# Performance work log

Measured on AMD Instinct MI355X. Metric: run time of the kernel, lower is better.

The kernel has to match this reference:

```python
import jax, jax.numpy as jnp
import numpy as np

N_HEAD = 16


def setup_inputs() -> dict:
    key = jax.random.key(0)
    k1, k2, k3 = jax.random.split(key, 3)
    B, T, N = 4, 2048, 1024
    x = jax.random.normal(k1, (B, T, N), dtype=jnp.float32)
    W_attn = jax.random.normal(k2, (N, 3 * N), dtype=jnp.float32) * (1.0 / np.sqrt(N))
    b_attn = jnp.zeros((3 * N,), dtype=jnp.float32)
    W_proj = jax.random.normal(k3, (N, N), dtype=jnp.float32) * (1.0 / np.sqrt(N))
    b_proj = jnp.zeros((N,), dtype=jnp.float32)
    return {"x": x, "W_attn": W_attn, "b_attn": b_attn, "W_proj": W_proj, "b_proj": b_proj}


def reference(x, W_attn, b_attn, W_proj, b_proj):
    B, T, N = x.shape
    H = N_HEAD
    Dh = N // H
    qkv = x @ W_attn + b_attn                      # [B, T, 3N]
    q, k, v = jnp.split(qkv, 3, axis=2)
    # [B, H, T, Dh]
    q = q.reshape(B, T, H, Dh).transpose(0, 2, 1, 3)
    k = k.reshape(B, T, H, Dh).transpose(0, 2, 1, 3)
    v = v.reshape(B, T, H, Dh).transpose(0, 2, 1, 3)
    att = jnp.einsum('bhqd,bhkd->bhqk', q, k) / (Dh ** 0.5)
    mask = jnp.tril(jnp.ones((T, T), dtype=bool))
    att = jnp.where(mask[None, None], att, jnp.finfo(x.dtype).min)
    att = jax.nn.softmax(att, axis=-1)
    y = jnp.einsum('bhqk,bhkd->bhqd', att, v)      # [B, H, T, Dh]
    y = y.transpose(0, 2, 1, 3).reshape(B, T, N)
    return y @ W_proj + b_proj
```

## Files before the change

kernel.cpp:

```cpp
#include <hip/hip_runtime.h>
#include <hip/hip_bf16.h>


typedef __attribute__((ext_vector_type(8))) short short8;
typedef __attribute__((ext_vector_type(4))) float f32x4;

#define MFMA16(a, b, c) __builtin_amdgcn_mfma_f32_16x16x32_bf16((a), (b), (c), 0, 0, 0)

#if defined(__has_builtin)
#if __has_builtin(__builtin_amdgcn_exp2f)
#define EXP2(x) __builtin_amdgcn_exp2f(x)
#endif
#endif
#ifndef EXP2
#define EXP2(x) exp2f(x)
#endif

__device__ __forceinline__ void gload_lds16(const void* g, void* l) {
  __builtin_amdgcn_global_load_lds(
      (const __attribute__((address_space(1))) unsigned int*)g,
      (__attribute__((address_space(3))) unsigned int*)l, 16, 0, 0);
}

__device__ __forceinline__ unsigned pack_bf16x2(float lo, float hi) {
  unsigned ulo = __float_as_uint(lo) + 0x8000u;
  unsigned uhi = __float_as_uint(hi) + 0x8000u;
  return __builtin_amdgcn_perm(uhi, ulo, 0x07060302u);
}

__device__ __forceinline__ unsigned short bf16u(float f) {
  return (unsigned short)((__float_as_uint(f) + 0x8000u) >> 16);
}

__global__ void conv_f32_bf16(const float* __restrict__ src,
                              unsigned* __restrict__ dst, int n4) {
  int i = blockIdx.x * blockDim.x + threadIdx.x;
  if (i >= n4) return;
  float4 v = ((const float4*)src)[i];
  uint2 o;
  o.x = pack_bf16x2(v.x, v.y);
  o.y = pack_bf16x2(v.z, v.w);
  ((uint2*)dst)[i] = o;
}

__global__ void transpose_bf16(const float* __restrict__ src,
                               __hip_bfloat16* __restrict__ dst, int R, int C) {
  __shared__ float tile[32][33];
  int tx = threadIdx.x, ty = threadIdx.y;
  int c0 = blockIdx.x * 32, r0 = blockIdx.y * 32;
#pragma unroll
  for (int i = 0; i < 32; i += 8)
    tile[ty + i][tx] = src[(long)(r0 + ty + i) * C + c0 + tx];
  __syncthreads();
#pragma unroll
  for (int i = 0; i < 32; i += 8)
    dst[(long)(c0 + ty + i) * R + r0 + tx] = __float2bfloat16(tile[tx][ty + i]);
}

template <int EPI>
__global__ __launch_bounds__(256, 2) void gemm_bt(
    const __hip_bfloat16* __restrict__ A, const __hip_bfloat16* __restrict__ Bt,
    const float* __restrict__ bias, void* o0, void* o1, void* o2, int N, int K) {
  __shared__ alignas(16) char smem[34816];
  short8 (*As)[8] = (short8(*)[8])smem;
  short8 (*Bs)[8] = (short8(*)[8])(smem + 16384);
  unsigned short (*C16)[136] = (unsigned short(*)[136])smem;
  float (*C32)[132] = (float(*)[132])smem;

  const int tid = threadIdx.x;
  const int lane = tid & 63, w = tid >> 6;
  const int l15 = lane & 15, quad = lane >> 4;
  const int wm = (w >> 1) * 64, wn = (w & 1) * 64;
  const int rowBase = blockIdx.y * 128;
  const int colBase = blockIdx.x * 128;
  const int sr8 = lane >> 3;
  const int scc = (lane & 7) ^ sr8;

  f32x4 acc[4][4];
#pragma unroll
  for (int mi = 0; mi < 4; ++mi)
#pragma unroll
    for (int ni = 0; ni < 4; ++ni)
      acc[mi][ni] = {0.f, 0.f, 0.f, 0.f};

  for (int k0 = 0; k0 < K; k0 += 64) {
    __syncthreads();
#pragma unroll
    for (int p = 0; p < 4; ++p) {
      const int rb = p * 32 + w * 8;
      const int row = rb + sr8;
      gload_lds16(A + (rowBase + row) * K + k0 + scc * 8, &As[rb][0]);
      gload_lds16(Bt + (colBase + row) * K + k0 + scc * 8, &Bs[rb][0]);
    }
    __syncthreads();
#pragma unroll
    for (int kc = 0; kc < 2; ++kc) {
      short8 af[4], bf[4];
#pragma unroll
      for (int mi = 0; mi < 4; ++mi) {
        int row = wm + mi * 16 + l15;
        af[mi] = As[row][(kc * 4 + quad) ^ (row & 7)];
      }
#pragma unroll
      for (int ni = 0; ni < 4; ++ni) {
        int row = wn + ni * 16 + l15;
        bf[ni] = Bs[row][(kc * 4 + quad) ^ (row & 7)];
      }
#pragma unroll
      for (int mi = 0; mi < 4; ++mi)
#pragma unroll
        for (int ni = 0; ni < 4; ++ni)
          acc[mi][ni] = MFMA16(af[mi], bf[ni], acc[mi][ni]);
    }
  }

  float bcol[4];
#pragma unroll
  for (int ni = 0; ni < 4; ++ni) bcol[ni] = bias[colBase + wn + ni * 16 + l15];

  if (EPI == 0) {
    const int which = colBase >> 10;
    const int b = rowBase >> 11;
    const int tt0 = rowBase & 2047;
    const int n1base = colBase & 1023;
    __syncthreads();
    if (which != 2) {
#pragma unroll
      for (int mi = 0; mi < 4; ++mi)
#pragma unroll
        for (int ni = 0; ni < 4; ++ni)
#pragma unroll
          for (int r = 0; r < 4; ++r)
            C16[wm + mi * 16 + quad * 4 + r][wn + ni * 16 + l15] =
                bf16u(acc[mi][ni][r] + bcol[ni]);
    } else {
#pragma unroll
      for (int mi = 0; mi < 4; ++mi)
#pragma unroll
        for (int ni = 0; ni < 4; ++ni)
#pragma unroll
          for (int r = 0; r < 4; ++r)
            C16[wn + ni * 16 + l15][wm + mi * 16 + quad * 4 + r] =
                bf16u(acc[mi][ni][r] + bcol[ni]);
    }
    __syncthreads();
    unsigned short* o = (unsigned short*)(which == 0 ? o0 : which == 1 ? o1 : o2);
    if (which != 2) {
#pragma unroll
      for (int j = 0; j < 8; ++j) {
        int flat = j * 256 + tid;
        int trow = flat >> 4, ch = flat & 15;
        int h = (n1base + ((ch & 8) << 3)) >> 6;
        long addr = ((long)((b * 16 + h) * 2048 + tt0 + trow)) * 64 + (ch & 7) * 8;
        *(short8*)&o[addr] = *(const short8*)&C16[trow][ch * 8];
      }
    } else {
#pragma unroll
      for (int j = 0; j < 8; ++j) {
        int flat = j * 256 + tid;
        int dcol = flat >> 4, ch = flat & 15;
        int h = (n1base + (dcol & 64)) >> 6;
        long addr = ((long)((b * 16 + h) * 64 + (dcol & 63))) * 2048 + tt0 + ch * 8;
        *(short8*)&o[addr] = *(const short8*)&C16[dcol][ch * 8];
      }
    }
  } else {
    float* out = (float*)o0;
    for (int p = 0; p < 2; ++p) {
      __syncthreads();
      if ((w >> 1) == p) {
#pragma unroll
        for (int mi = 0; mi < 4; ++mi)
#pragma unroll
          for (int ni = 0; ni < 4; ++ni)
#pragma unroll
            for (int r = 0; r < 4; ++r)
              C32[mi * 16 + quad * 4 + r][wn + ni * 16 + l15] =
                  acc[mi][ni][r] + bcol[ni];
      }
      __syncthreads();
#pragma unroll
      for (int j = 0; j < 8; ++j) {
        int flat = j * 256 + tid;
        int row = flat >> 5, ch = flat & 31;
        float4 v4 = *(const float4*)&C32[row][ch * 4];
        *(float4*)&out[(long)(rowBase + p * 64 + row) * N + colBase + ch * 4] = v4;
      }
    }
  }
}

__global__ __launch_bounds__(512, 6) void attn_kernel(
    const __hip_bfloat16* __restrict__ Q, const __hip_bfloat16* __restrict__ K,
    const __hip_bfloat16* __restrict__ Vt, __hip_bfloat16* __restrict__ Y, int T) {
  __shared__ short8 Ks[2][64][8];
  __shared__ short8 Vs[2][64][8];
  __shared__ alignas(16) unsigned short Pl[8][16][72];
  const int tid = threadIdx.x;
  const int w = tid >> 6, lane = tid & 63, l15 = lane & 15, quad = lane >> 4;
  const int bh = blockIdx.y;
  const int b = bh >> 4, h = bh & 15;
  const int qb = gridDim.x - 1 - blockIdx.x;
  const int qrow0 = qb * 128 + w * 16;
  const __hip_bfloat16* Qp = Q + (long)bh * T * 64;
  const __hip_bfloat16* Kp = K + (long)bh * T * 64;
  const __hip_bfloat16* Vp = Vt + (long)bh * 64 * T;

  const int sr8 = lane >> 3;
  const int sdc = lane & 7;

  short8 q0 = *(const short8*)(Qp + (qrow0 + l15) * 64 + quad * 8);
  short8 q1 = *(const short8*)(Qp + (qrow0 + l15) * 64 + 32 + quad * 8);

  f32x4 oacc[4];
#pragma unroll
  for (int g = 0; g < 4; ++g) oacc[g] = {0.f, 0.f, 0.f, 0.f};
  float l = 0.f;
  const float cscale = 0.125f * 1.44269504089f;
  const float Coff = 20.0f * 1.44269504089f;
  const int myq = qrow0 + l15;
  const int nkt = 2 * qb + 2;
  const int my_nkt = 2 * qb + 1 + (w >> 2);
  const int my_diag = my_nkt - 1;
  const int rsw = l15 & 7;

#define STAGE_ATTN(buf, kbase)                                              \
  do {                                                                      \
    const int rb = w * 8;                                                   \
    const int row = rb + sr8;                                               \
    const int cc = sdc ^ sr8;                                               \
    gload_lds16(Kp + ((kbase) + row) * 64 + cc * 8, &Ks[buf][rb][0]);       \
    gload_lds16(Vp + (long)row * T + (kbase) + cc * 8, &Vs[buf][rb][0]);    \
  } while (0)

  STAGE_ATTN(0, 0);
  __syncthreads();

  for (int kt = 0; kt < nkt; ++kt) {
    const int bb = kt & 1;
    const int kb = kt * 64;
    if (kt + 1 < nkt) STAGE_ATTN(bb ^ 1, kb + 64);

    if (kt < my_nkt) {
      f32x4 st[4];
#pragma unroll
      for (int g = 0; g < 4; ++g) {
        short8 k0 = Ks[bb][g * 16 + l15][quad ^ rsw];
        short8 k1 = Ks[bb][g * 16 + l15][(4 + quad) ^ rsw];
        f32x4 z = {0.f, 0.f, 0.f, 0.f};
        z = MFMA16(k0, q0, z);
        z = MFMA16(k1, q1, z);
        st[g] = z;
      }
      if (kt == my_diag) {
#pragma unroll
        for (int g = 0; g < 4; ++g)
#pragma unroll
          for (int r = 0; r < 4; ++r) {
            int key = kb + g * 16 + quad * 4 + r;
            if (key > myq) st[g][r] = -INFINITY;
          }
      }
      float p[16];
#pragma unroll
      for (int i = 0; i < 16; ++i)
        p[i] = EXP2(fmaf(st[i >> 2][i & 3], cscale, -Coff));
#pragma unroll
      for (int i = 0; i < 16; ++i) l += p[i];
#pragma unroll
      for (int g = 0; g < 4; ++g) {
        uint2 pk;
        pk.x = pack_bf16x2(p[g * 4 + 0], p[g * 4 + 1]);
        pk.y = pack_bf16x2(p[g * 4 + 2], p[g * 4 + 3]);
        *(uint2*)&Pl[w][l15][g * 16 + quad * 4] = pk;
      }
      short8 pb0 = *(short8*)&Pl[w][l15][quad * 8];
      short8 pb1 = *(short8*)&Pl[w][l15][32 + quad * 8];
#pragma unroll
      for (int g = 0; g < 4; ++g) {
        short8 v0 = Vs[bb][g * 16 + l15][quad ^ rsw];
        short8 v1 = Vs[bb][g * 16 + l15][(4 + quad) ^ rsw];
        oacc[g] = MFMA16(v0, pb0, oacc[g]);
        oacc[g] = MFMA16(v1, pb1, oacc[g]);
      }
    }
    __syncthreads();
  }

  l += __shfl_xor(l, 16);
  l += __shfl_xor(l, 32);

  const float inv = 1.0f / l;
  unsigned short* Yu = (unsigned short*)Y;
  const long rowoff = ((long)(b * 2048 + qrow0 + l15)) * 1024 + h * 64;
#pragma unroll
  for (int g = 0; g < 4; ++g) {
    uint2 o;
    o.x = pack_bf16x2(oacc[g][0] * inv, oacc[g][1] * inv);
    o.y = pack_bf16x2(oacc[g][2] * inv, oacc[g][3] * inv);
    *(uint2*)&Yu[rowoff + g * 16 + quad * 4] = o;
  }
}

extern "C" void kernel_launch(void* const* d_in, const int* in_sizes, int n_in,
                              void* d_out, int out_size, void* d_ws, size_t ws_size,
                              hipStream_t stream) {
  const float* x  = (const float*)d_in[0];
  const float* Wa = (const float*)d_in[1];
  const float* ba = (const float*)d_in[2];
  const float* Wp = (const float*)d_in[3];
  const float* bp = (const float*)d_in[4];
  float* out = (float*)d_out;

  char* ws = (char*)d_ws;
  __hip_bfloat16* Xb  = (__hip_bfloat16*)(ws);
  __hip_bfloat16* WaT = (__hip_bfloat16*)(ws + 16777216);
  __hip_bfloat16* WpT = (__hip_bfloat16*)(ws + 23068672);
  __hip_bfloat16* Qb  = (__hip_bfloat16*)(ws + 25165824);
  __hip_bfloat16* Kb  = (__hip_bfloat16*)(ws + 41943040);
  __hip_bfloat16* Vtb = (__hip_bfloat16*)(ws + 58720256);
  __hip_bfloat16* Yb  = (__hip_bfloat16*)(ws + 75497472);
  if (ws_size < 92274688) return;

  conv_f32_bf16<<<8192, 256, 0, stream>>>(x, (unsigned*)Xb, 2097152);
  transpose_bf16<<<dim3(96, 32), dim3(32, 8), 0, stream>>>(Wa, WaT, 1024, 3072);
  transpose_bf16<<<dim3(32, 32), dim3(32, 8), 0, stream>>>(Wp, WpT, 1024, 1024);
  gemm_bt<0><<<dim3(24, 64), 256, 0, stream>>>(Xb, WaT, ba, Qb, Kb, Vtb, 3072, 1024);
  attn_kernel<<<dim3(16, 64), 512, 0, stream>>>(Qb, Kb, Vtb, Yb, 2048);
  gemm_bt<1><<<dim3(8, 64), 256, 0, stream>>>(Yb, WpT, bp, out, nullptr, nullptr, 1024, 1024);
}
```

Baseline: 264.8 us.

## Switch attention to 32x32 MFMA with register-resident P via permlane32 swap

Rewrites the attention kernel to use 32x32x16 bf16 MFMAs with 4 waves, each covering 32 query rows. The P matrix is converted to the B-operand layout in registers with permlane32_swap, which removes the LDS round trip for P. The grid is flattened into a 1D launch with an interleaved query-tile order meant to balance causal work across the schedule. The block shrinks from 512 to 256 threads, so each wave does more work per K tile and occupancy changes.

```diff
diff --git a/kernel.cpp b/kernel.cpp
--- a/kernel.cpp
+++ b/kernel.cpp
@@ -4,8 +4,10 @@
 
 typedef __attribute__((ext_vector_type(8))) short short8;
 typedef __attribute__((ext_vector_type(4))) float f32x4;
+typedef __attribute__((ext_vector_type(16))) float f32x16;
 
 #define MFMA16(a, b, c) __builtin_amdgcn_mfma_f32_16x16x32_bf16((a), (b), (c), 0, 0, 0)
+#define MFMA32(a, b, c) __builtin_amdgcn_mfma_f32_32x32x16_bf16((a), (b), (c), 0, 0, 0)
 
 #if defined(__has_builtin)
 #if __has_builtin(__builtin_amdgcn_exp2f)
@@ -190,47 +192,58 @@
   }
 }
 
-__global__ __launch_bounds__(512, 6) void attn_kernel(
+__global__ __launch_bounds__(256, 4) void attn_kernel(
     const __hip_bfloat16* __restrict__ Q, const __hip_bfloat16* __restrict__ K,
     const __hip_bfloat16* __restrict__ Vt, __hip_bfloat16* __restrict__ Y, int T) {
   __shared__ short8 Ks[2][64][8];
   __shared__ short8 Vs[2][64][8];
-  __shared__ alignas(16) unsigned short Pl[8][16][72];
   const int tid = threadIdx.x;
-  const int w = tid >> 6, lane = tid & 63, l15 = lane & 15, quad = lane >> 4;
-  const int bh = blockIdx.y;
+  const int w = tid >> 6, lane = tid & 63;
+  const int c31 = lane & 31, half = lane >> 5;
+  const int rsw = c31 & 7;
+  const int idx = blockIdx.x;
+  const int bh = idx & 63;
   const int b = bh >> 4, h = bh & 15;
-  const int qb = gridDim.x - 1 - blockIdx.x;
-  const int qrow0 = qb * 128 + w * 16;
+  const int qsel = idx >> 6;
+  const int qq = qsel >> 2, qp = qsel & 3;
+  const int jt = (qq == 0) ? 15 - qp : (qq == 1) ? 8 + qp : (qq == 2) ? 4 + qp : 3 - qp;
+
+  const int qrow0 = jt * 128 + w * 32;
   const __hip_bfloat16* Qp = Q + (long)bh * T * 64;
   const __hip_bfloat16* Kp = K + (long)bh * T * 64;
   const __hip_bfloat16* Vp = Vt + (long)bh * 64 * T;
 
   const int sr8 = lane >> 3;
-  const int sdc = lane & 7;
-
-  short8 q0 = *(const short8*)(Qp + (qrow0 + l15) * 64 + quad * 8);
-  short8 q1 = *(const short8*)(Qp + (qrow0 + l15) * 64 + 32 + quad * 8);
-
-  f32x4 oacc[4];
-#pragma unroll
-  for (int g = 0; g < 4; ++g) oacc[g] = {0.f, 0.f, 0.f, 0.f};
-  float l = 0.f;
+  const int scc = (lane & 7) ^ sr8;
+
+  short8 qf[4];
+#pragma unroll
+  for (int s = 0; s < 4; ++s)
+    qf[s] = *(const short8*)(Qp + (qrow0 + c31) * 64 + s * 16 + half * 8);
+
+  f32x16 oacc[2];
+#pragma unroll
+  for (int g = 0; g < 2; ++g)
+#pragma unroll
+    for (int i = 0; i < 16; ++i) oacc[g][i] = 0.f;
+  float lsum = 0.f;
   const float cscale = 0.125f * 1.44269504089f;
   const float Coff = 20.0f * 1.44269504089f;
-  const int myq = qrow0 + l15;
-  const int nkt = 2 * qb + 2;
-  const int my_nkt = 2 * qb + 1 + (w >> 2);
+  const int myq = qrow0 + c31;
+  const int nkt = 2 * jt + 2;
+  const int my_nkt = 2 * jt + 1 + (w >> 1);
   const int my_diag = my_nkt - 1;
-  const int rsw = l15 & 7;
-
-#define STAGE_ATTN(buf, kbase)                                              \
-  do {                                                                      \
-    const int rb = w * 8;                                                   \
-    const int row = rb + sr8;                                               \
-    const int cc = sdc ^ sr8;                                               \
-    gload_lds16(Kp + ((kbase) + row) * 64 + cc * 8, &Ks[buf][rb][0]);       \
-    gload_lds16(Vp + (long)row * T + (kbase) + cc * 8, &Vs[buf][rb][0]);    \
+
+#define STAGE_ATTN(buf, kbase)                                                 \
+  do {                                                                         \
+    const int rb_ = w * 16;                                                    \
+    gload_lds16(Kp + ((kbase) + rb_ + sr8) * 64 + scc * 8, &Ks[buf][rb_][0]);  \
+    gload_lds16(Kp + ((kbase) + rb_ + 8 + sr8) * 64 + scc * 8,                 \
+                &Ks[buf][rb_ + 8][0]);                                         \
+    gload_lds16(Vp + (long)(rb_ + sr8) * T + (kbase) + scc * 8,                \
+                &Vs[buf][rb_][0]);                                             \
+    gload_lds16(Vp + (long)(rb_ + 8 + sr8) * T + (kbase) + scc * 8,            \
+                &Vs[buf][rb_ + 8][0]);                                         \
   } while (0)
 
   STAGE_ATTN(0, 0);
@@ -242,64 +255,68 @@
     if (kt + 1 < nkt) STAGE_ATTN(bb ^ 1, kb + 64);
 
     if (kt < my_nkt) {
-      f32x4 st[4];
-#pragma unroll
-      for (int g = 0; g < 4; ++g) {
-        short8 k0 = Ks[bb][g * 16 + l15][quad ^ rsw];
-        short8 k1 = Ks[bb][g * 16 + l15][(4 + quad) ^ rsw];
-        f32x4 z = {0.f, 0.f, 0.f, 0.f};
-        z = MFMA16(k0, q0, z);
-        z = MFMA16(k1, q1, z);
-        st[g] = z;
-      }
-      if (kt == my_diag) {
-#pragma unroll
-        for (int g = 0; g < 4; ++g)
-#pragma unroll
-          for (int r = 0; r < 4; ++r) {
-            int key = kb + g * 16 + quad * 4 + r;
-            if (key > myq) st[g][r] = -INFINITY;
+      short8 pb[4];
+#pragma unroll
+      for (int g = 0; g < 2; ++g) {
+        f32x16 z;
+#pragma unroll
+        for (int i = 0; i < 16; ++i) z[i] = 0.f;
+#pragma unroll
+        for (int s = 0; s < 4; ++s) {
+          short8 af = Ks[bb][g * 32 + c31][(s * 2 + half) ^ rsw];
+          z = MFMA32(af, qf[s], z);
+        }
+        if (kt == my_diag) {
+#pragma unroll
+          for (int r = 0; r < 16; ++r) {
+            int key = kb + g * 32 + (r & 3) + 8 * (r >> 2) + 4 * half;
+            if (key > myq) z[r] = -INFINITY;
           }
-      }
-      float p[16];
-#pragma unroll
-      for (int i = 0; i < 16; ++i)
-        p[i] = EXP2(fmaf(st[i >> 2][i & 3], cscale, -Coff));
-#pragma unroll
-      for (int i = 0; i < 16; ++i) l += p[i];
-#pragma unroll
-      for (int g = 0; g < 4; ++g) {
-        uint2 pk;
-        pk.x = pack_bf16x2(p[g * 4 + 0], p[g * 4 + 1]);
-        pk.y = pack_bf16x2(p[g * 4 + 2], p[g * 4 + 3]);
-        *(uint2*)&Pl[w][l15][g * 16 + quad * 4] = pk;
-      }
-      short8 pb0 = *(short8*)&Pl[w][l15][quad * 8];
-      short8 pb1 = *(short8*)&Pl[w][l15][32 + quad * 8];
-#pragma unroll
-      for (int g = 0; g < 4; ++g) {
-        short8 v0 = Vs[bb][g * 16 + l15][quad ^ rsw];
-        short8 v1 = Vs[bb][g * 16 + l15][(4 + quad) ^ rsw];
-        oacc[g] = MFMA16(v0, pb0, oacc[g]);
-        oacc[g] = MFMA16(v1, pb1, oacc[g]);
-      }
+        }
+        unsigned pk[8];
+#pragma unroll
+        for (int i = 0; i < 8; ++i) {
+          float p0 = EXP2(fmaf(z[2 * i], cscale, -Coff));
+          float p1 = EXP2(fmaf(z[2 * i + 1], cscale, -Coff));
+          lsum += p0 + p1;
+          pk[i] = pack_bf16x2(p0, p1);
+        }
+#pragma unroll
+        for (int s = 0; s < 2; ++s) {
+          auto r0 = __builtin_amdgcn_permlane32_swap(pk[4 * s + 0], pk[4 * s + 2],
+                                                     false, false);
+          auto r1 = __builtin_amdgcn_permlane32_swap(pk[4 * s + 1], pk[4 * s + 3],
+                                                     false, false);
+          union { unsigned u[4]; short8 s8; } cv;
+          cv.u[0] = r0[0]; cv.u[1] = r1[0]; cv.u[2] = r0[1]; cv.u[3] = r1[1];
+          pb[g * 2 + s] = cv.s8;
+        }
+      }
+#pragma unroll
+      for (int dg = 0; dg < 2; ++dg)
+#pragma unroll
+        for (int S = 0; S < 4; ++S) {
+          short8 vf = Vs[bb][dg * 32 + c31][(S * 2 + half) ^ rsw];
+          oacc[dg] = MFMA32(vf, pb[S], oacc[dg]);
+        }
     }
     __syncthreads();
   }
 
-  l += __shfl_xor(l, 16);
-  l += __shfl_xor(l, 32);
-
-  const float inv = 1.0f / l;
+  lsum += __shfl_xor(lsum, 32);
+
+  const float inv = 1.0f / lsum;
   unsigned short* Yu = (unsigned short*)Y;
-  const long rowoff = ((long)(b * 2048 + qrow0 + l15)) * 1024 + h * 64;
-#pragma unroll
-  for (int g = 0; g < 4; ++g) {
-    uint2 o;
-    o.x = pack_bf16x2(oacc[g][0] * inv, oacc[g][1] * inv);
-    o.y = pack_bf16x2(oacc[g][2] * inv, oacc[g][3] * inv);
-    *(uint2*)&Yu[rowoff + g * 16 + quad * 4] = o;
-  }
+  const long rowoff = ((long)(b * 2048 + qrow0 + c31)) * 1024 + h * 64;
+#pragma unroll
+  for (int dg = 0; dg < 2; ++dg)
+#pragma unroll
+    for (int rg = 0; rg < 4; ++rg) {
+      uint2 o;
+      o.x = pack_bf16x2(oacc[dg][rg * 4 + 0] * inv, oacc[dg][rg * 4 + 1] * inv);
+      o.y = pack_bf16x2(oacc[dg][rg * 4 + 2] * inv, oacc[dg][rg * 4 + 3] * inv);
+      *(uint2*)&Yu[rowoff + dg * 32 + half * 4 + rg * 8] = o;
+    }
 }
 
 extern "C" void kernel_launch(void* const* d_in, const int* in_sizes, int n_in,
@@ -326,6 +343,6 @@
   transpose_bf16<<<dim3(96, 32), dim3(32, 8), 0, stream>>>(Wa, WaT, 1024, 3072);
   transpose_bf16<<<dim3(32, 32), dim3(32, 8), 0, stream>>>(Wp, WpT, 1024, 1024);
   gemm_bt<0><<<dim3(24, 64), 256, 0, stream>>>(Xb, WaT, ba, Qb, Kb, Vtb, 3072, 1024);
-  attn_kernel<<<dim3(16, 64), 512, 0, stream>>>(Qb, Kb, Vtb, Yb, 2048);
+  attn_kernel<<<dim3(1024), dim3(256), 0, stream>>>(Qb, Kb, Vtb, Yb, 2048);
   gemm_bt<1><<<dim3(8, 64), 256, 0, stream>>>(Yb, WpT, bp, out, nullptr, nullptr, 1024, 1024);
 }
```

Result: faster. 228.8 us (-13.6%).
